# Kernel tuning notes

Hardware: AMD Instinct MI355X
Metric: run time of the kernel (lower is better)

## Reference

```python
import jax, jax.numpy as jnp
import numpy as np

B, S, H, R, K, L = 8, 2048, 512, 7, 10, 4
OFFSETS = np.array([-3, -2, -1, 1, 2, 3], dtype=np.int32)
BN_EPS = 1e-5


def setup_inputs() -> dict:
    key = jax.random.key(0)
    ks = jax.random.split(key, 12)
    u = lambda k, shape, s: jax.random.uniform(k, shape, minval=-s, maxval=s, dtype=jnp.float32)
    s3, sh, shr = 1.0 / np.sqrt(3.0), 1.0 / np.sqrt(H), 1.0 / np.sqrt(R * H)
    return {
        "n_coords": jax.random.normal(ks[0], (B, S, 3), jnp.float32),
        "ca_coords": jax.random.normal(ks[1], (B, S, 3), jnp.float32),
        "c_coords": jax.random.normal(ks[2], (B, S, 3), jnp.float32),
        "Wp": u(ks[3], (H, 3), s3),
        "bp": u(ks[4], (H,), s3),
        "Wlin": u(ks[5], (L, H, R * H), shr),
        "blin": u(ks[6], (L, H), shr),
        "Wself": u(ks[7], (L, H, H), sh),
        "bself": u(ks[8], (L, H), sh),
        "bn_gamma": jnp.ones((L, H), jnp.float32),
        "bn_beta": jnp.zeros((L, H), jnp.float32),
        "bn_mean": jax.random.normal(ks[9], (L, H), jnp.float32) * 0.1,
        "bn_var": jax.random.uniform(ks[10], (L, H), minval=0.5, maxval=1.5, dtype=jnp.float32),
    }


def _edges(pos):
    """Edge list per graph: sequential offsets -3..3 -> relations 0..5, KNN(k=10) -> relation 6."""
    i = jnp.arange(S)
    off = jnp.asarray(OFFSETS)
    dst_seq = i[:, None] + off[None, :]                            # [S,6]
    valid = (dst_seq >= 0) & (dst_seq < S)
    src_seq = jnp.broadcast_to(i[:, None], (S, 6))
    rel_seq = jnp.broadcast_to(jnp.arange(6, dtype=jnp.int32)[None, :], (S, 6))
    dst_seq = jnp.clip(dst_seq, 0, S - 1)
    # squared distances give the same topk-smallest ordering as torch.norm
    d2 = jnp.sum((pos[:, None, :] - pos[None, :, :]) ** 2, axis=-1)  # [S,S]
    _, knn = jax.lax.top_k(-d2, K + 1)                             # k+1 smallest, self first
    dst_knn = knn[:, 1:]                                           # drop self
    src_knn = jnp.broadcast_to(i[:, None], (S, K))
    rel_knn = jnp.full((S, K), 6, dtype=jnp.int32)
    src = jnp.concatenate([src_seq.reshape(-1), src_knn.reshape(-1)])
    dst = jnp.concatenate([dst_seq.reshape(-1), dst_knn.reshape(-1)])
    rel = jnp.concatenate([rel_seq.reshape(-1), rel_knn.reshape(-1)])
    w = jnp.concatenate([valid.reshape(-1).astype(pos.dtype),
                         jnp.ones((S * K,), pos.dtype)])
    return src, dst, rel, w


def _gearnet(ca_coords, Wp, bp, Wlin, blin, Wself, bself, bn_gamma, bn_beta, bn_mean, bn_var):
    def per_graph(pos):
        src, dst, rel, w = _edges(pos)
        seg = dst * R + rel                                        # node_out*num_relation + relation
        h = pos @ Wp.T + bp                                        # coord_projection: Linear(3, H)
        for l in range(L):
            msg = h[src] * w[:, None]                              # [E,H] gather + edge weight
            upd = jax.ops.segment_sum(msg, seg, num_segments=S * R)  # scatter-add per (node, relation)
            upd = upd.reshape(S, R * H)
            out = upd @ Wlin[l].T + blin[l] + h @ Wself[l].T + bself[l]
            out = (out - bn_mean[l]) * jax.lax.rsqrt(bn_var[l] + BN_EPS) * bn_gamma[l] + bn_beta[l]
            h = jax.nn.relu(out) + h                               # relu then short_cut residual
        return h
    return jax.vmap(per_graph)(ca_coords)                          # [B,S,H]


def reference(n_coords, ca_coords, c_coords, Wp, bp, Wlin, blin, Wself, bself,
              bn_gamma, bn_beta, bn_mean, bn_var):
    # n_coords / c_coords are accepted but unused, exactly as in the original forward.
    return _gearnet(ca_coords, Wp, bp, Wlin, blin, Wself, bself,
                    bn_gamma, bn_beta, bn_mean, bn_var)
```

## Files before the change

kernel.cpp:

```cpp
#include <hip/hip_runtime.h>
#include <stdint.h>

#define B_ 8
#define S_ 2048
#define H_ 512
#define R_ 7
#define K_ 10
#define L_ 4
#define KT_ 4096
#define RH_ 3584

typedef __attribute__((ext_vector_type(8))) short bf16x8;
typedef __attribute__((ext_vector_type(4))) float f32x4;
typedef __attribute__((ext_vector_type(4))) unsigned short u16x4;
typedef unsigned long long u64;

__device__ __forceinline__ unsigned short f2bf(float f){
  unsigned int u = __float_as_uint(f);
  u = (u + 0x7fffu + ((u >> 16) & 1u)) >> 16;
  return (unsigned short)u;
}

__device__ __forceinline__ float bf2f(unsigned short s){
  return __uint_as_float(((unsigned int)s) << 16);
}

__device__ __forceinline__ f32x4 bf4load(const unsigned short* p){
  u16x4 v = *(const u16x4*)p;
  f32x4 o;
#pragma unroll
  for (int e = 0; e < 4; e++) o[e] = bf2f(v[e]);
  return o;
}

__device__ __forceinline__ void gload16(const void* g, void* lds){
  __builtin_amdgcn_global_load_lds(
      (const __attribute__((address_space(1))) unsigned int*)g,
      (__attribute__((address_space(3))) unsigned int*)lds, 16, 0, 0);
}

__global__ __launch_bounds__(256) void knn_kernel(const float* __restrict__ pos,
                                                  int* __restrict__ knn){
  __shared__ float4 p4[S_];
  int b = blockIdx.y;
  const float* p = pos + (size_t)b * S_ * 3;
  for (int idx = threadIdx.x; idx < S_; idx += 256){
    float4 v; v.x = p[idx*3+0]; v.y = p[idx*3+1]; v.z = p[idx*3+2]; v.w = 0.f;
    p4[idx] = v;
  }
  __syncthreads();
  int w = threadIdx.x >> 6, l = threadIdx.x & 63;
  int i = blockIdx.x * 4 + w;
  float4 pi = p4[i];
  float xi = pi.x, yi = pi.y, zi = pi.z;
  u64 best[10];
#pragma unroll
  for (int q = 0; q < 10; q++) best[q] = ~0ull;
  for (int j = l; j < S_; j += 64){
    if (j == i) continue;
    float4 pj = p4[j];
    float dx = __fsub_rn(xi, pj.x);
    float dy = __fsub_rn(yi, pj.y);
    float dz = __fsub_rn(zi, pj.z);
    float d2 = __fadd_rn(__fadd_rn(__fmul_rn(dx,dx), __fmul_rn(dy,dy)), __fmul_rn(dz,dz));
    u64 key = ((u64)__float_as_uint(d2) << 32) | (unsigned)j;
    if (key < best[9]){
      best[9] = key;
#pragma unroll
      for (int q = 9; q > 0; --q){
        u64 a = best[q-1], c = best[q];
        u64 lo = a < c ? a : c, hi = a < c ? c : a;
        best[q-1] = lo; best[q] = hi;
      }
    }
  }
  int* out = knn + ((size_t)b * S_ + i) * K_;
#pragma unroll
  for (int t = 0; t < 10; t++){
    u64 cand = best[0];
    u64 m = cand;
#pragma unroll
    for (int o = 32; o; o >>= 1){
      u64 other = __shfl_xor(m, o);
      if (other < m) m = other;
    }
    if (cand == m){
#pragma unroll
      for (int q = 0; q < 9; q++) best[q] = best[q+1];
      best[9] = ~0ull;
    }
    if (l == 0) out[t] = (int)(unsigned)(m & 0xffffffffu);
  }
}

__global__ void count_kernel(const int* __restrict__ knn, int* __restrict__ counts){
  int idx = blockIdx.x * 256 + threadIdx.x;
  int b = idx / (S_ * K_);
  int d = knn[idx];
  atomicAdd(&counts[b * S_ + d], 1);
}

__global__ __launch_bounds__(256) void scan_kernel(const int* __restrict__ counts,
                                                   int* __restrict__ row_start,
                                                   int* __restrict__ cursor){
  __shared__ int lds[256];
  int b = blockIdx.x, t = threadIdx.x;
  int base = b * S_;
  int v[8]; int s = 0;
#pragma unroll
  for (int e = 0; e < 8; e++){ v[e] = s; s += counts[base + t*8 + e]; }
  lds[t] = s;
  __syncthreads();
  int total = s;
  for (int o = 1; o < 256; o <<= 1){
    int add = 0;
    if (t >= o) add = lds[t - o];
    __syncthreads();
    lds[t] += add;
    __syncthreads();
  }
  int ex = lds[t] - total;
  int rb = b * (S_ + 1);
#pragma unroll
  for (int e = 0; e < 8; e++){
    int val = ex + v[e];
    row_start[rb + t*8 + e] = val;
    cursor[base + t*8 + e] = val;
  }
  if (t == 255) row_start[rb + S_] = lds[255];
}

__global__ void fill_kernel(const int* __restrict__ knn, int* __restrict__ cursor,
                            int* __restrict__ col){
  int idx = blockIdx.x * 256 + threadIdx.x;
  int b = idx / (S_ * K_);
  int i = (idx / K_) % S_;
  int d = knn[idx];
  int p = atomicAdd(&cursor[b * S_ + d], 1);
  col[(size_t)b * S_ * K_ + p] = i;
}

__global__ void sort_kernel(const int* __restrict__ row_start, int* __restrict__ col){
  int idx = blockIdx.x * 256 + threadIdx.x;
  int b = idx / S_, d = idx % S_;
  int rs = row_start[b*(S_+1)+d], re = row_start[b*(S_+1)+d+1];
  int* c = col + (size_t)b * S_ * K_;
  for (int a = rs + 1; a < re; ++a){
    int vv = c[a]; int q = a - 1;
    while (q >= rs && c[q] > vv){ c[q+1] = c[q]; --q; }
    c[q+1] = vv;
  }
}

__global__ void prepw_kernel(const float* __restrict__ Wlin, const float* __restrict__ Wself,
                             unsigned short* __restrict__ Wt){
  size_t e = ((size_t)blockIdx.x * 256 + threadIdx.x) * 8;
  int k = (int)(e & 4095);
  int j = (int)((e >> 12) & 511);
  int l = (int)(e >> 21);
  const float* src = (k < RH_) ? Wlin + ((size_t)l * H_ + j) * RH_ + k
                               : Wself + ((size_t)l * H_ + j) * H_ + (k - RH_);
  union { unsigned short s[8]; uint4 u; } pk;
#pragma unroll
  for (int t = 0; t < 8; t++) pk.s[t] = f2bf(src[t]);
  *(uint4*)&Wt[e] = pk.u;
}

__global__ void prepa_kernel(const float* __restrict__ gam, const float* __restrict__ bet,
                             const float* __restrict__ mean, const float* __restrict__ var,
                             const float* __restrict__ blin, const float* __restrict__ bself,
                             float* __restrict__ scale, float* __restrict__ shift){
  int idx = blockIdx.x * 256 + threadIdx.x;
  float sc = gam[idx] * rsqrtf(var[idx] + 1e-5f);
  scale[idx] = sc;
  shift[idx] = bet[idx] + (blin[idx] + bself[idx] - mean[idx]) * sc;
}

__global__ void inith_kernel(const float* __restrict__ pos, const float* __restrict__ Wp,
                             const float* __restrict__ bp, float* __restrict__ h,
                             unsigned short* __restrict__ hb){
  int idx = blockIdx.x * 256 + threadIdx.x;
  int j = (idx & 127) * 4;
  int bs = idx >> 7;
  const float* p = pos + (size_t)bs * 3;
  float x = p[0], y = p[1], z = p[2];
  f32x4 o;
#pragma unroll
  for (int e = 0; e < 4; e++){
    const float* wr = Wp + (j + e) * 3;
    o[e] = x * wr[0] + y * wr[1] + z * wr[2] + bp[j + e];
  }
  *(f32x4*)&h[(size_t)bs * H_ + j] = o;
  unsigned int w0 = f2bf(o[0]) | ((unsigned)f2bf(o[1]) << 16);
  unsigned int w1 = f2bf(o[2]) | ((unsigned)f2bf(o[3]) << 16);
  uint2 u; u.x = w0; u.y = w1;
  *(uint2*)&hb[(size_t)bs * H_ + j] = u;
}

__global__ __launch_bounds__(128) void hknn_kernel(const unsigned short* __restrict__ hb,
                                                   const int* __restrict__ row_start,
                                                   const int* __restrict__ col,
                                                   unsigned short* __restrict__ hk){
  int bx = blockIdx.x;
  int d = (bx & 7) * 256 + (bx >> 3);
  int b = blockIdx.y;
  int j = threadIdx.x * 4;
  int rs = row_start[b * (S_ + 1) + d];
  int re = row_start[b * (S_ + 1) + d + 1];
  const int* cl = col + (size_t)b * S_ * K_;
  f32x4 acc = {0.f, 0.f, 0.f, 0.f};
  for (int e = rs; e < re; ++e){
    int i = cl[e];
    acc += bf4load(&hb[((size_t)b * S_ + i) * H_ + j]);
  }
  u16x4 v;
#pragma unroll
  for (int e = 0; e < 4; e++) v[e] = f2bf(acc[e]);
  *(u16x4*)&hk[((size_t)b * S_ + d) * H_ + j] = v;
}

__global__ __launch_bounds__(512) void gemmf_kernel(
    const unsigned short* __restrict__ hbin,
    const unsigned short* __restrict__ hkn,
    const unsigned short* __restrict__ Wt,
    float* __restrict__ h,
    unsigned short* __restrict__ hbout,
    const float* __restrict__ scale,
    const float* __restrict__ shift,
    const unsigned short* __restrict__ zbuf){
  __shared__ unsigned short As[3][128 * 64];
  __shared__ unsigned short Bs[3][256 * 64];
  int tid = threadIdx.x;
  int wg = blockIdx.x;
  int swz = (wg & 7) * 32 + (wg >> 3);
  int my = swz >> 1;
  int nx = swz & 1;
  int l = tid & 63, wid = tid >> 6;
  int wm = wid >> 2, wn = wid & 3;
  f32x4 acc[4][4] = {};

  int arow = tid >> 3;
  int lA8 = ((tid & 7) ^ (arow & 7)) << 3;
  int gr0 = my * 128 + arow, gr1 = gr0 + 64;
  const unsigned short* Bp0 = Wt + (size_t)(nx * 256 +   0 + arow) * KT_ + lA8;
  const unsigned short* Bp1 = Wt + (size_t)(nx * 256 +  64 + arow) * KT_ + lA8;
  const unsigned short* Bp2 = Wt + (size_t)(nx * 256 + 128 + arow) * KT_ + lA8;
  const unsigned short* Bp3 = Wt + (size_t)(nx * 256 + 192 + arow) * KT_ + lA8;
  const unsigned short *sa0, *sa1;

#define SETSLC(rr) do {                                                       \
    int _r = (rr);                                                            \
    const unsigned short *_b0, *_b1;                                          \
    if (_r < 6){                                                              \
      int _sh = (_r < 3) ? (3 - _r) : (2 - _r);          \
      int _s0 = gr0 + _sh, _s1 = gr1 + _sh;                                   \
      _b0 = (((unsigned)_s0 >> 11) == ((unsigned)gr0 >> 11)) ? hbin + (size_t)_s0 * H_ : zbuf; \
      _b1 = (((unsigned)_s1 >> 11) == ((unsigned)gr1 >> 11)) ? hbin + (size_t)_s1 * H_ : zbuf; \
    } else {                                                                  \
      const unsigned short* _bb = (_r == 6) ? hkn : hbin;                     \
      _b0 = _bb + (size_t)gr0 * H_; _b1 = _bb + (size_t)gr1 * H_;             \
    }                                                                         \
    sa0 = _b0 + lA8; sa1 = _b1 + lA8;                                         \
  } while (0)

  int dA0 = tid * 8, dA1 = (512 + tid) * 8;
  int dB0 = tid * 8, dB1 = (512 + tid) * 8, dB2 = (1024 + tid) * 8, dB3 = (1536 + tid) * 8;

#define STAGE(sl, ko, kb) do {                             \
    gload16(sa0 + (ko), &As[sl][dA0]);                     \
    gload16(sa1 + (ko), &As[sl][dA1]);                     \
    gload16(Bp0 + (kb), &Bs[sl][dB0]);                     \
    gload16(Bp1 + (kb), &Bs[sl][dB1]);                     \
    gload16(Bp2 + (kb), &Bs[sl][dB2]);                     \
    gload16(Bp3 + (kb), &Bs[sl][dB3]);                     \
  } while (0)

  SETSLC(0);
  STAGE(0, 0, 0);
  STAGE(1, 64, 64);

  int kcr = l >> 4, lr = l & 15, lr7 = l & 7;
  int rA0 = wm * 64 + lr, rB0 = wn * 64 + lr;
  int pc0 = (kcr ^ lr7) * 8;
  int pc1 = ((4 + kcr) ^ lr7) * 8;
  int s = 0;
#pragma unroll 1
  for (int t = 0; t < 64; ++t){
    int s2 = s + 2; if (s2 >= 3) s2 -= 3;
    int tt = t + 2;
    bool st = (t < 62);
    if (st) SETSLC(tt >> 3);

    if (t < 63) asm volatile("s_waitcnt vmcnt(6)" ::: "memory");
    else        asm volatile("s_waitcnt vmcnt(0)" ::: "memory");
    __builtin_amdgcn_s_barrier();
    asm volatile("" ::: "memory");

    bf16x8 af0[4], af1[4], bf0[4], bf1[4];
#pragma unroll
    for (int mi = 0; mi < 4; mi++){
      af0[mi] = *(const bf16x8*)&As[s][(rA0 + mi * 16) * 64 + pc0];
      af1[mi] = *(const bf16x8*)&As[s][(rA0 + mi * 16) * 64 + pc1];
    }
#pragma unroll
    for (int ni = 0; ni < 4; ni++){
      bf0[ni] = *(const bf16x8*)&Bs[s][(rB0 + ni * 16) * 64 + pc0];
      bf1[ni] = *(const bf16x8*)&Bs[s][(rB0 + ni * 16) * 64 + pc1];
    }
    if (st) STAGE(s2, (tt & 7) * 64, tt * 64);

    asm volatile("s_waitcnt lgkmcnt(0)" ::: "memory");
    __builtin_amdgcn_sched_barrier(0);
    __builtin_amdgcn_s_setprio(1);
#pragma unroll
    for (int mi = 0; mi < 4; mi++)
#pragma unroll
      for (int ni = 0; ni < 4; ni++){
        acc[mi][ni] = __builtin_amdgcn_mfma_f32_16x16x32_bf16(af0[mi], bf0[ni], acc[mi][ni], 0, 0, 0);
        acc[mi][ni] = __builtin_amdgcn_mfma_f32_16x16x32_bf16(af1[mi], bf1[ni], acc[mi][ni], 0, 0, 0);
      }
    __builtin_amdgcn_s_setprio(0);
    asm volatile("" ::: "memory");
    __builtin_amdgcn_s_barrier();
    asm volatile("" ::: "memory");
    ++s; if (s == 3) s = 0;
  }
#undef STAGE
#undef SETSLC

  int r0 = (l >> 4) * 4, c0 = l & 15;
#pragma unroll
  for (int ni = 0; ni < 4; ni++){
    int gcol = nx * 256 + wn * 64 + ni * 16 + c0;
    float sc = scale[gcol], sf = shift[gcol];
#pragma unroll
    for (int mi = 0; mi < 4; mi++){
#pragma unroll
      for (int reg = 0; reg < 4; reg++){
        int grow = my * 128 + wm * 64 + mi * 16 + r0 + reg;
        size_t o = (size_t)grow * H_ + gcol;
        float val = fmaxf(acc[mi][ni][reg] * sc + sf, 0.f);
        float hv = h[o] + val;
        h[o] = hv;
        hbout[o] = f2bf(hv);
      }
    }
  }
}

extern "C" void kernel_launch(void* const* d_in, const int* in_sizes, int n_in,
                              void* d_out, int out_size, void* d_ws, size_t ws_size,
                              hipStream_t stream){
  const float* ca    = (const float*)d_in[1];
  const float* Wp    = (const float*)d_in[3];
  const float* bp    = (const float*)d_in[4];
  const float* Wlin  = (const float*)d_in[5];
  const float* blin  = (const float*)d_in[6];
  const float* Wself = (const float*)d_in[7];
  const float* bself = (const float*)d_in[8];
  const float* gam   = (const float*)d_in[9];
  const float* bet   = (const float*)d_in[10];
  const float* mean  = (const float*)d_in[11];
  const float* var   = (const float*)d_in[12];
  float* h = (float*)d_out;

  char* ws = (char*)d_ws;
  size_t off = 0;
  auto alloc = [&](size_t bytes) -> char* {
    char* p = ws + off;
    off = (off + bytes + 255) & ~(size_t)255;
    return p;
  };
  int* knn       = (int*)alloc((size_t)B_ * S_ * K_ * 4);
  int* counts    = (int*)alloc((size_t)B_ * S_ * 4);
  int* row_start = (int*)alloc((size_t)B_ * (S_ + 1) * 4);
  int* cursor    = (int*)alloc((size_t)B_ * S_ * 4);
  int* col       = (int*)alloc((size_t)B_ * S_ * K_ * 4);
  unsigned short* Wt  = (unsigned short*)alloc((size_t)L_ * H_ * KT_ * 2);
  float* scale   = (float*)alloc((size_t)L_ * H_ * 4);
  float* shift   = (float*)alloc((size_t)L_ * H_ * 4);
  unsigned short* hbA = (unsigned short*)alloc((size_t)B_ * S_ * H_ * 2);
  unsigned short* hbB = (unsigned short*)alloc((size_t)B_ * S_ * H_ * 2);
  unsigned short* hkn = (unsigned short*)alloc((size_t)B_ * S_ * H_ * 2);
  unsigned short* zbuf = (unsigned short*)alloc(4096 * 2);

  hipMemsetAsync(counts, 0, (size_t)B_ * S_ * 4, stream);
  hipMemsetAsync(zbuf, 0, 4096 * 2, stream);
  knn_kernel<<<dim3(S_ / 4, B_), 256, 0, stream>>>(ca, knn);
  count_kernel<<<dim3(B_ * S_ * K_ / 256), 256, 0, stream>>>(knn, counts);
  scan_kernel<<<dim3(B_), 256, 0, stream>>>(counts, row_start, cursor);
  fill_kernel<<<dim3(B_ * S_ * K_ / 256), 256, 0, stream>>>(knn, cursor, col);
  sort_kernel<<<dim3(B_ * S_ / 256), 256, 0, stream>>>(row_start, col);
  prepw_kernel<<<dim3((int)((size_t)L_ * H_ * KT_ / 8 / 256)), 256, 0, stream>>>(Wlin, Wself, Wt);
  prepa_kernel<<<dim3(L_ * H_ / 256), 256, 0, stream>>>(gam, bet, mean, var, blin, bself, scale, shift);
  inith_kernel<<<dim3(B_ * S_ * (H_ / 4) / 256), 256, 0, stream>>>(ca, Wp, bp, h, hbA);

  for (int l = 0; l < L_; l++){
    unsigned short* in  = (l & 1) ? hbB : hbA;
    unsigned short* out = (l & 1) ? hbA : hbB;
    hknn_kernel<<<dim3(S_, B_), 128, 0, stream>>>(in, row_start, col, hkn);
    gemmf_kernel<<<dim3(256), 512, 0, stream>>>(
        in, hkn, Wt + (size_t)l * H_ * KT_, h, out,
        scale + l * H_, shift + l * H_, zbuf);
  }
}
```

Baseline: 565.1 us.

## Halve GEMM waves to four with 128x64 per-wave tiles; batch KNN rows per wave

The fused GEMM kernel now runs 256 threads (4 waves) instead of 512. Each wave covers all 128 rows and 64 columns with a 8x4 MFMA accumulator tile, so more work is done per LDS fragment load. The K-step is split into two MFMA halves, with the second-half LDS reads overlapping the first-half MFMAs, and the A-source pointers are recomputed only when the relation slice changes. The KNN kernel processes 4 query points per wave with a quarter of the blocks, which cuts the redundant LDS fill of positions. The trade-off is higher register pressure from 128 accumulators and fewer waves to hide latency.

```diff
diff --git a/kernel.cpp b/kernel.cpp
--- a/kernel.cpp
+++ b/kernel.cpp
@@ -50,46 +50,49 @@
   }
   __syncthreads();
   int w = threadIdx.x >> 6, l = threadIdx.x & 63;
-  int i = blockIdx.x * 4 + w;
-  float4 pi = p4[i];
-  float xi = pi.x, yi = pi.y, zi = pi.z;
-  u64 best[10];
-#pragma unroll
-  for (int q = 0; q < 10; q++) best[q] = ~0ull;
-  for (int j = l; j < S_; j += 64){
-    if (j == i) continue;
-    float4 pj = p4[j];
-    float dx = __fsub_rn(xi, pj.x);
-    float dy = __fsub_rn(yi, pj.y);
-    float dz = __fsub_rn(zi, pj.z);
-    float d2 = __fadd_rn(__fadd_rn(__fmul_rn(dx,dx), __fmul_rn(dy,dy)), __fmul_rn(dz,dz));
-    u64 key = ((u64)__float_as_uint(d2) << 32) | (unsigned)j;
-    if (key < best[9]){
-      best[9] = key;
-#pragma unroll
-      for (int q = 9; q > 0; --q){
-        u64 a = best[q-1], c = best[q];
-        u64 lo = a < c ? a : c, hi = a < c ? c : a;
-        best[q-1] = lo; best[q] = hi;
+#pragma unroll 1
+  for (int q = 0; q < 4; ++q){
+    int i = blockIdx.x * 16 + w * 4 + q;
+    float4 pi = p4[i];
+    float xi = pi.x, yi = pi.y, zi = pi.z;
+    u64 best[10];
+#pragma unroll
+    for (int t = 0; t < 10; t++) best[t] = ~0ull;
+    for (int j = l; j < S_; j += 64){
+      if (j == i) continue;
+      float4 pj = p4[j];
+      float dx = __fsub_rn(xi, pj.x);
+      float dy = __fsub_rn(yi, pj.y);
+      float dz = __fsub_rn(zi, pj.z);
+      float d2 = __fadd_rn(__fadd_rn(__fmul_rn(dx,dx), __fmul_rn(dy,dy)), __fmul_rn(dz,dz));
+      u64 key = ((u64)__float_as_uint(d2) << 32) | (unsigned)j;
+      if (key < best[9]){
+        best[9] = key;
+#pragma unroll
+        for (int t = 9; t > 0; --t){
+          u64 a = best[t-1], c = best[t];
+          u64 lo = a < c ? a : c, hi = a < c ? c : a;
+          best[t-1] = lo; best[t] = hi;
+        }
       }
     }
-  }
-  int* out = knn + ((size_t)b * S_ + i) * K_;
-#pragma unroll
-  for (int t = 0; t < 10; t++){
-    u64 cand = best[0];
-    u64 m = cand;
-#pragma unroll
-    for (int o = 32; o; o >>= 1){
-      u64 other = __shfl_xor(m, o);
-      if (other < m) m = other;
+    int* out = knn + ((size_t)b * S_ + i) * K_;
+#pragma unroll
+    for (int t = 0; t < 10; t++){
+      u64 cand = best[0];
+      u64 m = cand;
+#pragma unroll
+      for (int o = 32; o; o >>= 1){
+        u64 other = __shfl_xor(m, o);
+        if (other < m) m = other;
+      }
+      if (cand == m){
+#pragma unroll
+        for (int qq = 0; qq < 9; qq++) best[qq] = best[qq+1];
+        best[9] = ~0ull;
+      }
+      if (l == 0) out[t] = (int)(unsigned)(m & 0xffffffffu);
     }
-    if (cand == m){
-#pragma unroll
-      for (int q = 0; q < 9; q++) best[q] = best[q+1];
-      best[9] = ~0ull;
-    }
-    if (l == 0) out[t] = (int)(unsigned)(m & 0xffffffffu);
   }
 }
 
@@ -219,7 +222,7 @@
   *(u16x4*)&hk[((size_t)b * S_ + d) * H_ + j] = v;
 }
 
-__global__ __launch_bounds__(512) void gemmf_kernel(
+__global__ __launch_bounds__(256, 1) void gemmf_kernel(
     const unsigned short* __restrict__ hbin,
     const unsigned short* __restrict__ hkn,
     const unsigned short* __restrict__ Wt,
@@ -235,44 +238,56 @@
   int swz = (wg & 7) * 32 + (wg >> 3);
   int my = swz >> 1;
   int nx = swz & 1;
-  int l = tid & 63, wid = tid >> 6;
-  int wm = wid >> 2, wn = wid & 3;
-  f32x4 acc[4][4] = {};
-
-  int arow = tid >> 3;
-  int lA8 = ((tid & 7) ^ (arow & 7)) << 3;
-  int gr0 = my * 128 + arow, gr1 = gr0 + 64;
-  const unsigned short* Bp0 = Wt + (size_t)(nx * 256 +   0 + arow) * KT_ + lA8;
-  const unsigned short* Bp1 = Wt + (size_t)(nx * 256 +  64 + arow) * KT_ + lA8;
-  const unsigned short* Bp2 = Wt + (size_t)(nx * 256 + 128 + arow) * KT_ + lA8;
-  const unsigned short* Bp3 = Wt + (size_t)(nx * 256 + 192 + arow) * KT_ + lA8;
-  const unsigned short *sa0, *sa1;
+  int l = tid & 63, wn = tid >> 6;
+  f32x4 acc[8][4] = {};
+
+  int r = tid >> 3;
+  int lA8 = ((tid & 7) ^ (r & 7)) << 3;
+  int gr0 = my * 128 + r,      gr1 = gr0 + 32,
+      gr2 = gr0 + 64,          gr3 = gr0 + 96;
+  const unsigned short* Bq0 = Wt + (size_t)(nx * 256 + r +   0) * KT_ + lA8;
+  const unsigned short* Bq1 = Wt + (size_t)(nx * 256 + r +  32) * KT_ + lA8;
+  const unsigned short* Bq2 = Wt + (size_t)(nx * 256 + r +  64) * KT_ + lA8;
+  const unsigned short* Bq3 = Wt + (size_t)(nx * 256 + r +  96) * KT_ + lA8;
+  const unsigned short* Bq4 = Wt + (size_t)(nx * 256 + r + 128) * KT_ + lA8;
+  const unsigned short* Bq5 = Wt + (size_t)(nx * 256 + r + 160) * KT_ + lA8;
+  const unsigned short* Bq6 = Wt + (size_t)(nx * 256 + r + 192) * KT_ + lA8;
+  const unsigned short* Bq7 = Wt + (size_t)(nx * 256 + r + 224) * KT_ + lA8;
+  const unsigned short *sa0, *sa1, *sa2, *sa3;
 
 #define SETSLC(rr) do {                                                       \
     int _r = (rr);                                                            \
-    const unsigned short *_b0, *_b1;                                          \
     if (_r < 6){                                                              \
       int _sh = (_r < 3) ? (3 - _r) : (2 - _r);          \
-      int _s0 = gr0 + _sh, _s1 = gr1 + _sh;                                   \
-      _b0 = (((unsigned)_s0 >> 11) == ((unsigned)gr0 >> 11)) ? hbin + (size_t)_s0 * H_ : zbuf; \
-      _b1 = (((unsigned)_s1 >> 11) == ((unsigned)gr1 >> 11)) ? hbin + (size_t)_s1 * H_ : zbuf; \
+      int _s0 = gr0 + _sh, _s1 = gr1 + _sh, _s2 = gr2 + _sh, _s3 = gr3 + _sh; \
+      sa0 = (((unsigned)_s0 >> 11) == ((unsigned)gr0 >> 11)) ? hbin + (size_t)_s0 * H_ + lA8 : zbuf + lA8; \
+      sa1 = (((unsigned)_s1 >> 11) == ((unsigned)gr1 >> 11)) ? hbin + (size_t)_s1 * H_ + lA8 : zbuf + lA8; \
+      sa2 = (((unsigned)_s2 >> 11) == ((unsigned)gr2 >> 11)) ? hbin + (size_t)_s2 * H_ + lA8 : zbuf + lA8; \
+      sa3 = (((unsigned)_s3 >> 11) == ((unsigned)gr3 >> 11)) ? hbin + (size_t)_s3 * H_ + lA8 : zbuf + lA8; \
     } else {                                                                  \
       const unsigned short* _bb = (_r == 6) ? hkn : hbin;                     \
-      _b0 = _bb + (size_t)gr0 * H_; _b1 = _bb + (size_t)gr1 * H_;             \
+      sa0 = _bb + (size_t)gr0 * H_ + lA8;                                     \
+      sa1 = _bb + (size_t)gr1 * H_ + lA8;                                     \
+      sa2 = _bb + (size_t)gr2 * H_ + lA8;                                     \
+      sa3 = _bb + (size_t)gr3 * H_ + lA8;                                     \
     }                                                                         \
-    sa0 = _b0 + lA8; sa1 = _b1 + lA8;                                         \
   } while (0)
 
-  int dA0 = tid * 8, dA1 = (512 + tid) * 8;
-  int dB0 = tid * 8, dB1 = (512 + tid) * 8, dB2 = (1024 + tid) * 8, dB3 = (1536 + tid) * 8;
-
-#define STAGE(sl, ko, kb) do {                             \
-    gload16(sa0 + (ko), &As[sl][dA0]);                     \
-    gload16(sa1 + (ko), &As[sl][dA1]);                     \
-    gload16(Bp0 + (kb), &Bs[sl][dB0]);                     \
-    gload16(Bp1 + (kb), &Bs[sl][dB1]);                     \
-    gload16(Bp2 + (kb), &Bs[sl][dB2]);                     \
-    gload16(Bp3 + (kb), &Bs[sl][dB3]);                     \
+  int dA0 = tid * 8, dA1 = (tid + 256) * 8, dA2 = (tid + 512) * 8, dA3 = (tid + 768) * 8;
+
+#define STAGE(sl, ka, kb) do {                             \
+    gload16(sa0 + (ka), &As[sl][dA0]);                     \
+    gload16(sa1 + (ka), &As[sl][dA1]);                     \
+    gload16(sa2 + (ka), &As[sl][dA2]);                     \
+    gload16(sa3 + (ka), &As[sl][dA3]);                     \
+    gload16(Bq0 + (kb), &Bs[sl][dA0]);                     \
+    gload16(Bq1 + (kb), &Bs[sl][dA1]);                     \
+    gload16(Bq2 + (kb), &Bs[sl][dA2]);                     \
+    gload16(Bq3 + (kb), &Bs[sl][dA3]);                     \
+    gload16(Bq4 + (kb), &Bs[sl][(tid + 1024) * 8]);        \
+    gload16(Bq5 + (kb), &Bs[sl][(tid + 1280) * 8]);        \
+    gload16(Bq6 + (kb), &Bs[sl][(tid + 1536) * 8]);        \
+    gload16(Bq7 + (kb), &Bs[sl][(tid + 1792) * 8]);        \
   } while (0)
 
   SETSLC(0);
@@ -280,7 +295,8 @@
   STAGE(1, 64, 64);
 
   int kcr = l >> 4, lr = l & 15, lr7 = l & 7;
-  int rA0 = wm * 64 + lr, rB0 = wn * 64 + lr;
+  int rA0 = lr;
+  int rB0 = wn * 64 + lr;
   int pc0 = (kcr ^ lr7) * 8;
   int pc1 = ((4 + kcr) ^ lr7) * 8;
   int s = 0;
@@ -289,36 +305,49 @@
     int s2 = s + 2; if (s2 >= 3) s2 -= 3;
     int tt = t + 2;
     bool st = (t < 62);
-    if (st) SETSLC(tt >> 3);
-
-    if (t < 63) asm volatile("s_waitcnt vmcnt(6)" ::: "memory");
+    if (st && (tt & 7) == 0) SETSLC(tt >> 3);
+
+    if (t < 63) asm volatile("s_waitcnt vmcnt(12)" ::: "memory");
     else        asm volatile("s_waitcnt vmcnt(0)" ::: "memory");
     __builtin_amdgcn_s_barrier();
     asm volatile("" ::: "memory");
 
-    bf16x8 af0[4], af1[4], bf0[4], bf1[4];
-#pragma unroll
-    for (int mi = 0; mi < 4; mi++){
+    bf16x8 af0[8], af1[8], bf0[4], bf1[4];
+#pragma unroll
+    for (int mi = 0; mi < 8; mi++)
       af0[mi] = *(const bf16x8*)&As[s][(rA0 + mi * 16) * 64 + pc0];
+#pragma unroll
+    for (int ni = 0; ni < 4; ni++)
+      bf0[ni] = *(const bf16x8*)&Bs[s][(rB0 + ni * 16) * 64 + pc0];
+    __builtin_amdgcn_sched_barrier(0);
+#pragma unroll
+    for (int mi = 0; mi < 8; mi++)
       af1[mi] = *(const bf16x8*)&As[s][(rA0 + mi * 16) * 64 + pc1];
-    }
-#pragma unroll
-    for (int ni = 0; ni < 4; ni++){
-      bf0[ni] = *(const bf16x8*)&Bs[s][(rB0 + ni * 16) * 64 + pc0];
+#pragma unroll
+    for (int ni = 0; ni < 4; ni++)
       bf1[ni] = *(const bf16x8*)&Bs[s][(rB0 + ni * 16) * 64 + pc1];
-    }
+    __builtin_amdgcn_sched_barrier(0);
+
+    asm volatile("s_waitcnt lgkmcnt(12)" ::: "memory");
+    __builtin_amdgcn_sched_barrier(0);
+    __builtin_amdgcn_s_setprio(1);
+#pragma unroll
+    for (int mi = 0; mi < 8; mi++)
+#pragma unroll
+      for (int ni = 0; ni < 4; ni++)
+        acc[mi][ni] = __builtin_amdgcn_mfma_f32_16x16x32_bf16(af0[mi], bf0[ni], acc[mi][ni], 0, 0, 0);
+    __builtin_amdgcn_s_setprio(0);
+
     if (st) STAGE(s2, (tt & 7) * 64, tt * 64);
 
     asm volatile("s_waitcnt lgkmcnt(0)" ::: "memory");
     __builtin_amdgcn_sched_barrier(0);
     __builtin_amdgcn_s_setprio(1);
 #pragma unroll
-    for (int mi = 0; mi < 4; mi++)
-#pragma unroll
-      for (int ni = 0; ni < 4; ni++){
-        acc[mi][ni] = __builtin_amdgcn_mfma_f32_16x16x32_bf16(af0[mi], bf0[ni], acc[mi][ni], 0, 0, 0);
+    for (int mi = 0; mi < 8; mi++)
+#pragma unroll
+      for (int ni = 0; ni < 4; ni++)
         acc[mi][ni] = __builtin_amdgcn_mfma_f32_16x16x32_bf16(af1[mi], bf1[ni], acc[mi][ni], 0, 0, 0);
-      }
     __builtin_amdgcn_s_setprio(0);
     asm volatile("" ::: "memory");
     __builtin_amdgcn_s_barrier();
@@ -334,10 +363,10 @@
     int gcol = nx * 256 + wn * 64 + ni * 16 + c0;
     float sc = scale[gcol], sf = shift[gcol];
 #pragma unroll
-    for (int mi = 0; mi < 4; mi++){
+    for (int mi = 0; mi < 8; mi++){
 #pragma unroll
       for (int reg = 0; reg < 4; reg++){
-        int grow = my * 128 + wm * 64 + mi * 16 + r0 + reg;
+        int grow = my * 128 + mi * 16 + r0 + reg;
         size_t o = (size_t)grow * H_ + gcol;
         float val = fmaxf(acc[mi][ni][reg] * sc + sf, 0.f);
         float hv = h[o] + val;
@@ -386,7 +415,7 @@
 
   hipMemsetAsync(counts, 0, (size_t)B_ * S_ * 4, stream);
   hipMemsetAsync(zbuf, 0, 4096 * 2, stream);
-  knn_kernel<<<dim3(S_ / 4, B_), 256, 0, stream>>>(ca, knn);
+  knn_kernel<<<dim3(S_ / 16, B_), 256, 0, stream>>>(ca, knn);
   count_kernel<<<dim3(B_ * S_ * K_ / 256), 256, 0, stream>>>(knn, counts);
   scan_kernel<<<dim3(B_), 256, 0, stream>>>(counts, row_start, cursor);
   fill_kernel<<<dim3(B_ * S_ * K_ / 256), 256, 0, stream>>>(knn, cursor, col);
@@ -399,7 +428,7 @@
     unsigned short* in  = (l & 1) ? hbB : hbA;
     unsigned short* out = (l & 1) ? hbA : hbB;
     hknn_kernel<<<dim3(S_, B_), 128, 0, stream>>>(in, row_start, col, hkn);
-    gemmf_kernel<<<dim3(256), 512, 0, stream>>>(
+    gemmf_kernel<<<dim3(256), 256, 0, stream>>>(
         in, hkn, Wt + (size_t)l * H_ * KT_, h, out,
         scale + l * H_, shift + l * H_, zbuf);
   }
```

Result: slower. 683.5 us (+20.9%).

## Split GEMM k-step into two halves overlapping LDS reads with MFMA; batch knn queries per wave

Applied to the files above, without the earlier changes.

The GEMM inner loop now loads the first k-half fragments, waits on partial lgkmcnt, and issues its MFMAs while the second-half LDS reads are still in flight. The global stage issue moves between the two halves. Separately, each knn wave now handles four query points, so a block reloads the position table into LDS once per 16 queries instead of once per 4. The split schedule relies on the lgkmcnt count being right, and knn has fewer blocks and so less parallelism.

```diff
diff --git a/kernel.cpp b/kernel.cpp
--- a/kernel.cpp
+++ b/kernel.cpp
@@ -50,46 +50,49 @@
   }
   __syncthreads();
   int w = threadIdx.x >> 6, l = threadIdx.x & 63;
-  int i = blockIdx.x * 4 + w;
-  float4 pi = p4[i];
-  float xi = pi.x, yi = pi.y, zi = pi.z;
-  u64 best[10];
-#pragma unroll
-  for (int q = 0; q < 10; q++) best[q] = ~0ull;
-  for (int j = l; j < S_; j += 64){
-    if (j == i) continue;
-    float4 pj = p4[j];
-    float dx = __fsub_rn(xi, pj.x);
-    float dy = __fsub_rn(yi, pj.y);
-    float dz = __fsub_rn(zi, pj.z);
-    float d2 = __fadd_rn(__fadd_rn(__fmul_rn(dx,dx), __fmul_rn(dy,dy)), __fmul_rn(dz,dz));
-    u64 key = ((u64)__float_as_uint(d2) << 32) | (unsigned)j;
-    if (key < best[9]){
-      best[9] = key;
-#pragma unroll
-      for (int q = 9; q > 0; --q){
-        u64 a = best[q-1], c = best[q];
-        u64 lo = a < c ? a : c, hi = a < c ? c : a;
-        best[q-1] = lo; best[q] = hi;
+#pragma unroll 1
+  for (int q = 0; q < 4; ++q){
+    int i = blockIdx.x * 16 + w * 4 + q;
+    float4 pi = p4[i];
+    float xi = pi.x, yi = pi.y, zi = pi.z;
+    u64 best[10];
+#pragma unroll
+    for (int t = 0; t < 10; t++) best[t] = ~0ull;
+    for (int j = l; j < S_; j += 64){
+      if (j == i) continue;
+      float4 pj = p4[j];
+      float dx = __fsub_rn(xi, pj.x);
+      float dy = __fsub_rn(yi, pj.y);
+      float dz = __fsub_rn(zi, pj.z);
+      float d2 = __fadd_rn(__fadd_rn(__fmul_rn(dx,dx), __fmul_rn(dy,dy)), __fmul_rn(dz,dz));
+      u64 key = ((u64)__float_as_uint(d2) << 32) | (unsigned)j;
+      if (key < best[9]){
+        best[9] = key;
+#pragma unroll
+        for (int t = 9; t > 0; --t){
+          u64 a = best[t-1], c = best[t];
+          u64 lo = a < c ? a : c, hi = a < c ? c : a;
+          best[t-1] = lo; best[t] = hi;
+        }
       }
     }
-  }
-  int* out = knn + ((size_t)b * S_ + i) * K_;
-#pragma unroll
-  for (int t = 0; t < 10; t++){
-    u64 cand = best[0];
-    u64 m = cand;
-#pragma unroll
-    for (int o = 32; o; o >>= 1){
-      u64 other = __shfl_xor(m, o);
-      if (other < m) m = other;
+    int* out = knn + ((size_t)b * S_ + i) * K_;
+#pragma unroll
+    for (int t = 0; t < 10; t++){
+      u64 cand = best[0];
+      u64 m = cand;
+#pragma unroll
+      for (int o = 32; o; o >>= 1){
+        u64 other = __shfl_xor(m, o);
+        if (other < m) m = other;
+      }
+      if (cand == m){
+#pragma unroll
+        for (int qq = 0; qq < 9; qq++) best[qq] = best[qq+1];
+        best[9] = ~0ull;
+      }
+      if (l == 0) out[t] = (int)(unsigned)(m & 0xffffffffu);
     }
-    if (cand == m){
-#pragma unroll
-      for (int q = 0; q < 9; q++) best[q] = best[q+1];
-      best[9] = ~0ull;
-    }
-    if (l == 0) out[t] = (int)(unsigned)(m & 0xffffffffu);
   }
 }
 
@@ -298,15 +301,31 @@
 
     bf16x8 af0[4], af1[4], bf0[4], bf1[4];
 #pragma unroll
-    for (int mi = 0; mi < 4; mi++){
+    for (int mi = 0; mi < 4; mi++)
       af0[mi] = *(const bf16x8*)&As[s][(rA0 + mi * 16) * 64 + pc0];
+#pragma unroll
+    for (int ni = 0; ni < 4; ni++)
+      bf0[ni] = *(const bf16x8*)&Bs[s][(rB0 + ni * 16) * 64 + pc0];
+    __builtin_amdgcn_sched_barrier(0);
+#pragma unroll
+    for (int mi = 0; mi < 4; mi++)
       af1[mi] = *(const bf16x8*)&As[s][(rA0 + mi * 16) * 64 + pc1];
-    }
-#pragma unroll
-    for (int ni = 0; ni < 4; ni++){
-      bf0[ni] = *(const bf16x8*)&Bs[s][(rB0 + ni * 16) * 64 + pc0];
+#pragma unroll
+    for (int ni = 0; ni < 4; ni++)
       bf1[ni] = *(const bf16x8*)&Bs[s][(rB0 + ni * 16) * 64 + pc1];
-    }
+    __builtin_amdgcn_sched_barrier(0);
+
+    asm volatile("s_waitcnt lgkmcnt(8)" ::: "memory");
+    __builtin_amdgcn_sched_barrier(0);
+    __builtin_amdgcn_s_setprio(1);
+#pragma unroll
+    for (int mi = 0; mi < 4; mi++)
+#pragma unroll
+      for (int ni = 0; ni < 4; ni++)
+        acc[mi][ni] = __builtin_amdgcn_mfma_f32_16x16x32_bf16(af0[mi], bf0[ni], acc[mi][ni], 0, 0, 0);
+    __builtin_amdgcn_s_setprio(0);
+    __builtin_amdgcn_sched_barrier(0);
+
     if (st) STAGE(s2, (tt & 7) * 64, tt * 64);
 
     asm volatile("s_waitcnt lgkmcnt(0)" ::: "memory");
@@ -315,10 +334,8 @@
 #pragma unroll
     for (int mi = 0; mi < 4; mi++)
 #pragma unroll
-      for (int ni = 0; ni < 4; ni++){
-        acc[mi][ni] = __builtin_amdgcn_mfma_f32_16x16x32_bf16(af0[mi], bf0[ni], acc[mi][ni], 0, 0, 0);
+      for (int ni = 0; ni < 4; ni++)
         acc[mi][ni] = __builtin_amdgcn_mfma_f32_16x16x32_bf16(af1[mi], bf1[ni], acc[mi][ni], 0, 0, 0);
-      }
     __builtin_amdgcn_s_setprio(0);
     asm volatile("" ::: "memory");
     __builtin_amdgcn_s_barrier();
@@ -386,7 +403,7 @@
 
   hipMemsetAsync(counts, 0, (size_t)B_ * S_ * 4, stream);
   hipMemsetAsync(zbuf, 0, 4096 * 2, stream);
-  knn_kernel<<<dim3(S_ / 4, B_), 256, 0, stream>>>(ca, knn);
+  knn_kernel<<<dim3(S_ / 16, B_), 256, 0, stream>>>(ca, knn);
   count_kernel<<<dim3(B_ * S_ * K_ / 256), 256, 0, stream>>>(knn, counts);
   scan_kernel<<<dim3(B_), 256, 0, stream>>>(counts, row_start, cursor);
   fill_kernel<<<dim3(B_ * S_ * K_ / 256), 256, 0, stream>>>(knn, cursor, col);
```

Result: no change. 567.3 us (+0.4%).
